# Performance work log

Measured on AMD Instinct MI355X. Metric: run time of the kernel, lower is better.

Reference implementation:

```python
import jax, jax.numpy as jnp
import numpy as np

B, Q, K = 4, 256, 1024
Q_SIZE, K_SIZE, V_SIZE, H = 256, 256, 256, 128
NEG = -1000000.0


def setup_inputs() -> dict:
    key = jax.random.key(0)
    ks = jax.random.split(key, 7)
    return {
        "queries": jax.random.normal(ks[0], (B, Q, Q_SIZE), dtype=jnp.float32),
        "keys": jax.random.normal(ks[1], (B, K, K_SIZE), dtype=jnp.float32),
        "values": jax.random.normal(ks[2], (B, K, V_SIZE), dtype=jnp.float32),
        "valid_lens": jax.random.randint(ks[3], (B,), 1, K + 1),
        # Linear weights stored torch-style: [out_features, in_features]
        "W_q": jax.random.normal(ks[4], (H, Q_SIZE), dtype=jnp.float32) * (1.0 / np.sqrt(Q_SIZE)),
        "W_k": jax.random.normal(ks[5], (H, K_SIZE), dtype=jnp.float32) * (1.0 / np.sqrt(K_SIZE)),
        "w_v": jax.random.normal(ks[6], (H,), dtype=jnp.float32) * (1.0 / np.sqrt(H)),
    }


def reference(queries, keys, values, valid_lens, W_q, W_k, w_v):
    # Projections (torch Linear: x @ W.T)
    q = jnp.einsum("bqi,hi->bqh", queries, W_q)  # [B,Q,H]
    k = jnp.einsum("bki,hi->bkh", keys, W_k)     # [B,K,H]
    # Broadcast add + tanh -> additive scores via dot with w_v
    feat = jnp.tanh(q[:, :, None, :] + k[:, None, :, :])  # [B,Q,K,H]
    scores = jnp.einsum("bqkh,h->bqk", feat, w_v)          # [B,Q,K]
    # masked_softmax: 1-D valid_lens broadcast over all query rows
    mask = jnp.arange(K)[None, None, :] < valid_lens[:, None, None]  # [B,1,K]
    scores = jnp.where(mask, scores, NEG)
    attn = jax.nn.softmax(scores, axis=-1)
    # dropout p=0.0 (eval): identity
    return jnp.einsum("bqk,bkv->bqv", attn, values)  # [B,Q,V]
```

## Files before the change

kernel.cpp:

```cpp
#include <hip/hip_runtime.h>
#include <math.h>

#define BQ   4
#define QN   256
#define KN   1024
#define DIN  256
#define HD   128

#define C2F   2.8853900817779268f
#define NL2E  (-2.8853900817779268f)

__global__ __launch_bounds__(256, 2) void proj_kernel(const float* __restrict__ queries,
                                                      const float* __restrict__ keys,
                                                      const float* __restrict__ W_q,
                                                      const float* __restrict__ W_k,
                                                      float* __restrict__ Eq,
                                                      float* __restrict__ EkT4) {
    __shared__ float xT[32][18];
    __shared__ float WT[32][136];

    const int t = threadIdx.x;
    const int row0 = blockIdx.x * 16;
    const bool is_q = row0 < BQ * QN;
    const float* x = is_q ? queries : keys;
    const float* W = is_q ? W_q : W_k;
    const int xr0 = is_q ? row0 : row0 - BQ * QN;

    const int h0 = (t & 31) * 4;
    const int r0 = (t >> 5) * 2;

    float acc[2][4];
#pragma unroll
    for (int r = 0; r < 2; r++)
#pragma unroll
        for (int c = 0; c < 4; c++) acc[r][c] = 0.f;

    for (int ks = 0; ks < DIN; ks += 32) {
        __syncthreads();
        if (t < 128) {
            const int r = t >> 3, k4 = (t & 7) * 4;
            float4 xv = *(const float4*)(x + (size_t)(xr0 + r) * DIN + ks + k4);
            xT[k4 + 0][r] = xv.x; xT[k4 + 1][r] = xv.y;
            xT[k4 + 2][r] = xv.z; xT[k4 + 3][r] = xv.w;
        }
#pragma unroll
        for (int u = 0; u < 4; u++) {
            const int h = (t >> 3) + 32 * u, k4 = (t & 7) * 4;
            float4 wv = *(const float4*)(W + (size_t)h * DIN + ks + k4);
            WT[k4 + 0][h] = wv.x; WT[k4 + 1][h] = wv.y;
            WT[k4 + 2][h] = wv.z; WT[k4 + 3][h] = wv.w;
        }
        __syncthreads();
#pragma unroll
        for (int kk = 0; kk < 32; kk++) {
            float2 xv = *(const float2*)&xT[kk][r0];
            float4 wv = *(const float4*)&WT[kk][h0];
            const float xr[2] = {xv.x, xv.y};
            const float wc[4] = {wv.x, wv.y, wv.z, wv.w};
#pragma unroll
            for (int r = 0; r < 2; r++)
#pragma unroll
                for (int c = 0; c < 4; c++)
                    acc[r][c] = __builtin_fmaf(xr[r], wc[c], acc[r][c]);
        }
    }

    if (is_q) {
#pragma unroll
        for (int r = 0; r < 2; r++) {
            float4 o;
            o.x = __builtin_amdgcn_exp2f(C2F * acc[r][0]);
            o.y = __builtin_amdgcn_exp2f(C2F * acc[r][1]);
            o.z = __builtin_amdgcn_exp2f(C2F * acc[r][2]);
            o.w = __builtin_amdgcn_exp2f(C2F * acc[r][3]);
            *(float4*)(Eq + (size_t)(row0 + r0 + r) * HD + h0) = o;
        }
    } else {
        const int krow = row0 - BQ * QN;
        const int b = krow >> 10, k0 = (krow & (KN - 1)) + r0;
        const int h4 = t & 31;
#pragma unroll
        for (int r = 0; r < 2; r++) {
            float4 o;
            o.x = __builtin_amdgcn_exp2f(C2F * acc[r][0]);
            o.y = __builtin_amdgcn_exp2f(C2F * acc[r][1]);
            o.z = __builtin_amdgcn_exp2f(C2F * acc[r][2]);
            o.w = __builtin_amdgcn_exp2f(C2F * acc[r][3]);
            *(float4*)(EkT4 + ((size_t)(b * 32 + h4) * KN + k0 + r) * 4) = o;
        }
    }
}

__global__ __launch_bounds__(256, 4) void score_kernel(const float* __restrict__ Eq,
                                                       const float* __restrict__ EkT4,
                                                       const int* __restrict__ valid_lens,
                                                       const float* __restrict__ w_v,
                                                       float* __restrict__ attn,
                                                       float* __restrict__ partial) {
    __shared__ float s_w[HD];
    __shared__ float s_pq[HD][8];
    __shared__ float s_part[2][8][128];
    __shared__ float s_red[4][4];

    const int blk = blockIdx.x;
    const int b = blk & 3;
    const int q0 = ((blk >> 2) & 31) * 8;
    const int c = blk >> 7;
    const int t = threadIdx.x;
    const int valid = valid_lens[b];
    float* pp = partial + (size_t)(b * QN + q0) * 8;

    if (c * 128 >= valid) {
        if (t < 8) pp[t * 8 + c] = 0.f;
        return;
    }

    const int kl = t & 127;
    const int hh = t >> 7;
    const int k = c * 128 + kl;

    if (t < HD) s_w[t] = w_v[t];
    {
        const int h = t & 127;
#pragma unroll
        for (int j = 0; j < 4; j++) {
            const int q = (t >> 7) * 4 + j;
            s_pq[h][q] = Eq[(size_t)(b * QN + q0 + q) * HD + h];
        }
    }
    __syncthreads();

    const float4* kcol = (const float4*)EkT4 + ((size_t)(b * 32 + hh * 16) * KN + k);
    float acc[8] = {0.f, 0.f, 0.f, 0.f, 0.f, 0.f, 0.f, 0.f};

#pragma unroll 4
    for (int i = 0; i < 16; i++) {
        float4 ek4 = kcol[(size_t)i * KN];
        const int hb = hh * 64 + i * 4;
        const float ekv[4] = {ek4.x, ek4.y, ek4.z, ek4.w};
#pragma unroll
        for (int j = 0; j < 4; j++) {
            const float ek = ekv[j];
            const float w = s_w[hb + j];
            float4 p0 = *(const float4*)&s_pq[hb + j][0];
            float4 p1 = *(const float4*)&s_pq[hb + j][4];
            acc[0] = __builtin_fmaf(w, __builtin_amdgcn_rcpf(__builtin_fmaf(ek, p0.x, 1.0f)), acc[0]);
            acc[1] = __builtin_fmaf(w, __builtin_amdgcn_rcpf(__builtin_fmaf(ek, p0.y, 1.0f)), acc[1]);
            acc[2] = __builtin_fmaf(w, __builtin_amdgcn_rcpf(__builtin_fmaf(ek, p0.z, 1.0f)), acc[2]);
            acc[3] = __builtin_fmaf(w, __builtin_amdgcn_rcpf(__builtin_fmaf(ek, p0.w, 1.0f)), acc[3]);
            acc[4] = __builtin_fmaf(w, __builtin_amdgcn_rcpf(__builtin_fmaf(ek, p1.x, 1.0f)), acc[4]);
            acc[5] = __builtin_fmaf(w, __builtin_amdgcn_rcpf(__builtin_fmaf(ek, p1.y, 1.0f)), acc[5]);
            acc[6] = __builtin_fmaf(w, __builtin_amdgcn_rcpf(__builtin_fmaf(ek, p1.z, 1.0f)), acc[6]);
            acc[7] = __builtin_fmaf(w, __builtin_amdgcn_rcpf(__builtin_fmaf(ek, p1.w, 1.0f)), acc[7]);
        }
    }

#pragma unroll
    for (int q = 0; q < 8; q++) s_part[hh][q][kl] = acc[q];
    __syncthreads();

    const int qb = (t >> 7) * 4;
    float* arow = attn + (size_t)(b * QN + q0 + qb) * KN + k;
    float psum[4];
#pragma unroll
    for (int j = 0; j < 4; j++) {
        const int q = qb + j;
        float tot = s_part[0][q][kl] + s_part[1][q][kl];
        float e = (k < valid) ? __builtin_amdgcn_exp2f(NL2E * tot) : 0.f;
        arow[(size_t)j * KN] = e;
#pragma unroll
        for (int off = 32; off > 0; off >>= 1) e += __shfl_xor(e, off, 64);
        psum[j] = e;
    }
    const int wv = t >> 6;
    if ((t & 63) == 0) {
#pragma unroll
        for (int j = 0; j < 4; j++) s_red[wv][j] = psum[j];
    }
    __syncthreads();
    if (t < 8) {
        const int q = t;
        float s = (q < 4) ? (s_red[0][q] + s_red[1][q])
                          : (s_red[2][q - 4] + s_red[3][q - 4]);
        pp[q * 8 + c] = s;
    }
}

__global__ __launch_bounds__(256, 2) void av_kernel(const float* __restrict__ attn,
                                                    const float* __restrict__ partial,
                                                    const float* __restrict__ values,
                                                    const int* __restrict__ valid_lens,
                                                    float* __restrict__ out) {
    __shared__ float s_aT[32][20];
    __shared__ float s_v[32][36];
    __shared__ float s_red[8][16][37];
    __shared__ float s_inv[16];

    const int blk = blockIdx.x;
    const int b = blk & 3;
    const int qt = (blk >> 2) & 15;
    const int vt = blk >> 6;
    const int t = threadIdx.x;
    const int q0 = qt * 16, v0 = vt * 32;
    const int valid = valid_lens[b];
    const int T = (valid + 31) >> 5;

    if (t < 16) {
        const float* pr = partial + (size_t)(b * QN + q0 + t) * 8;
        float4 pA = *(const float4*)pr;
        float4 pB = *(const float4*)(pr + 4);
        s_inv[t] = 1.0f / (pA.x + pA.y + pA.z + pA.w + pB.x + pB.y + pB.z + pB.w);
    }

    const int sr = t >> 3, sc = (t & 7) * 4;
    const float* abase = attn + (size_t)(b * QN + q0 + (sr & 15)) * KN + sc;
    const float* vbase = values + ((size_t)b * KN + sr) * DIN + v0 + sc;

    const int ks = t >> 5;
    const int qh = (t >> 3) & 3;
    const int vh = t & 7;

    float acc[4][4];
#pragma unroll
    for (int r = 0; r < 4; r++)
#pragma unroll
        for (int c = 0; c < 4; c++) acc[r][c] = 0.f;

    float4 ra = *(const float4*)abase;
    float4 rv = *(const float4*)vbase;

    for (int tile = 0; tile < T; tile++) {
        __syncthreads();
        if (t < 128) {
            s_aT[sc + 0][sr] = ra.x;
            s_aT[sc + 1][sr] = ra.y;
            s_aT[sc + 2][sr] = ra.z;
            s_aT[sc + 3][sr] = ra.w;
        }
        *(float4*)&s_v[sr][sc] = rv;
        __syncthreads();
        if (tile + 1 < T) {
            ra = *(const float4*)(abase + (tile + 1) * 32);
            rv = *(const float4*)(vbase + (size_t)(tile + 1) * 32 * DIN);
        }
#pragma unroll
        for (int i = 0; i < 4; i++) {
            const int kk = ks * 4 + i;
            float4 aq = *(const float4*)&s_aT[kk][qh * 4];
            float4 vv = *(const float4*)&s_v[kk][vh * 4];
            const float ar[4] = {aq.x, aq.y, aq.z, aq.w};
            const float vc[4] = {vv.x, vv.y, vv.z, vv.w};
#pragma unroll
            for (int r = 0; r < 4; r++)
#pragma unroll
                for (int c = 0; c < 4; c++)
                    acc[r][c] = __builtin_fmaf(ar[r], vc[c], acc[r][c]);
        }
    }

#pragma unroll
    for (int r = 0; r < 4; r++)
        *(float4*)&s_red[ks][qh * 4 + r][vh * 4] =
            make_float4(acc[r][0], acc[r][1], acc[r][2], acc[r][3]);
    __syncthreads();

    if (t < 128) {
        const int q = t >> 3, v4 = (t & 7) * 4;
        float4 o = {0.f, 0.f, 0.f, 0.f};
#pragma unroll
        for (int s = 0; s < 8; s++) {
            float4 r = *(const float4*)&s_red[s][q][v4];
            o.x += r.x; o.y += r.y; o.z += r.z; o.w += r.w;
        }
        const float inv = s_inv[q];
        o.x *= inv; o.y *= inv; o.z *= inv; o.w *= inv;
        *(float4*)(out + (size_t)(b * QN + q0 + q) * DIN + v0 + v4) = o;
    }
}

extern "C" void kernel_launch(void* const* d_in, const int* in_sizes, int n_in,
                              void* d_out, int out_size, void* d_ws, size_t ws_size,
                              hipStream_t stream) {
    const float* queries    = (const float*)d_in[0];
    const float* keys       = (const float*)d_in[1];
    const float* values     = (const float*)d_in[2];
    const int*   valid_lens = (const int*)d_in[3];
    const float* W_q        = (const float*)d_in[4];
    const float* W_k        = (const float*)d_in[5];
    const float* w_v        = (const float*)d_in[6];
    float* out = (float*)d_out;

    float* Eq      = (float*)d_ws;
    float* EkT4    = Eq + (size_t)BQ * QN * HD;
    float* attn    = EkT4 + (size_t)BQ * HD * KN;
    float* partial = attn + (size_t)BQ * QN * KN;

    proj_kernel<<<(BQ * QN + BQ * KN) / 16, 256, 0, stream>>>(queries, keys, W_q, W_k, Eq, EkT4);
    score_kernel<<<BQ * (QN / 8) * 8, 256, 0, stream>>>(Eq, EkT4, valid_lens, w_v, attn, partial);
    av_kernel<<<BQ * 16 * 8, 256, 0, stream>>>(attn, partial, values, valid_lens, out);
}
```

Before: 111.9 us.

## Compact score grid over valid key chunks with 64-key blocks and 4-way H split

```diff
diff --git a/kernel.cpp b/kernel.cpp
--- a/kernel.cpp
+++ b/kernel.cpp
@@ -99,90 +99,79 @@
                                                        float* __restrict__ partial) {
     __shared__ float s_w[HD];
     __shared__ float s_pq[HD][8];
-    __shared__ float s_part[2][8][128];
-    __shared__ float s_red[4][4];
-
-    const int blk = blockIdx.x;
-    const int b = blk & 3;
-    const int q0 = ((blk >> 2) & 31) * 8;
-    const int c = blk >> 7;
+    __shared__ float s_part[4][8][64];
+
+    const int v0 = valid_lens[0], v1 = valid_lens[1];
+    const int v2 = valid_lens[2], v3 = valid_lens[3];
+    const int e0 = 32 * ((v0 + 63) >> 6);
+    const int e1 = e0 + 32 * ((v1 + 63) >> 6);
+    const int e2 = e1 + 32 * ((v2 + 63) >> 6);
+    const int e3 = e2 + 32 * ((v3 + 63) >> 6);
+    const int j = blockIdx.x;
+    if (j >= e3) return;
+    int b, valid, jj;
+    if (j < e0)      { b = 0; valid = v0; jj = j; }
+    else if (j < e1) { b = 1; valid = v1; jj = j - e0; }
+    else if (j < e2) { b = 2; valid = v2; jj = j - e1; }
+    else             { b = 3; valid = v3; jj = j - e2; }
+    const int q0 = (jj & 31) * 8;
+    const int c  = jj >> 5;
+
     const int t = threadIdx.x;
-    const int valid = valid_lens[b];
-    float* pp = partial + (size_t)(b * QN + q0) * 8;
-
-    if (c * 128 >= valid) {
-        if (t < 8) pp[t * 8 + c] = 0.f;
-        return;
-    }
-
-    const int kl = t & 127;
-    const int hh = t >> 7;
-    const int k = c * 128 + kl;
+    const int l = t & 63;
+    const int w = t >> 6;
+    const int k = c * 64 + l;
 
     if (t < HD) s_w[t] = w_v[t];
     {
         const int h = t & 127;
 #pragma unroll
-        for (int j = 0; j < 4; j++) {
-            const int q = (t >> 7) * 4 + j;
+        for (int jq = 0; jq < 4; jq++) {
+            const int q = (t >> 7) * 4 + jq;
             s_pq[h][q] = Eq[(size_t)(b * QN + q0 + q) * HD + h];
         }
     }
     __syncthreads();
 
-    const float4* kcol = (const float4*)EkT4 + ((size_t)(b * 32 + hh * 16) * KN + k);
+    const float4* kcol = (const float4*)EkT4 + ((size_t)(b * 32 + w * 8) * KN + k);
     float acc[8] = {0.f, 0.f, 0.f, 0.f, 0.f, 0.f, 0.f, 0.f};
 
-#pragma unroll 4
-    for (int i = 0; i < 16; i++) {
+#pragma unroll
+    for (int i = 0; i < 8; i++) {
         float4 ek4 = kcol[(size_t)i * KN];
-        const int hb = hh * 64 + i * 4;
+        const int hb = w * 32 + i * 4;
         const float ekv[4] = {ek4.x, ek4.y, ek4.z, ek4.w};
 #pragma unroll
-        for (int j = 0; j < 4; j++) {
-            const float ek = ekv[j];
-            const float w = s_w[hb + j];
-            float4 p0 = *(const float4*)&s_pq[hb + j][0];
-            float4 p1 = *(const float4*)&s_pq[hb + j][4];
-            acc[0] = __builtin_fmaf(w, __builtin_amdgcn_rcpf(__builtin_fmaf(ek, p0.x, 1.0f)), acc[0]);
-            acc[1] = __builtin_fmaf(w, __builtin_amdgcn_rcpf(__builtin_fmaf(ek, p0.y, 1.0f)), acc[1]);
-            acc[2] = __builtin_fmaf(w, __builtin_amdgcn_rcpf(__builtin_fmaf(ek, p0.z, 1.0f)), acc[2]);
-            acc[3] = __builtin_fmaf(w, __builtin_amdgcn_rcpf(__builtin_fmaf(ek, p0.w, 1.0f)), acc[3]);
-            acc[4] = __builtin_fmaf(w, __builtin_amdgcn_rcpf(__builtin_fmaf(ek, p1.x, 1.0f)), acc[4]);
-            acc[5] = __builtin_fmaf(w, __builtin_amdgcn_rcpf(__builtin_fmaf(ek, p1.y, 1.0f)), acc[5]);
-            acc[6] = __builtin_fmaf(w, __builtin_amdgcn_rcpf(__builtin_fmaf(ek, p1.z, 1.0f)), acc[6]);
-            acc[7] = __builtin_fmaf(w, __builtin_amdgcn_rcpf(__builtin_fmaf(ek, p1.w, 1.0f)), acc[7]);
-        }
-    }
-
-#pragma unroll
-    for (int q = 0; q < 8; q++) s_part[hh][q][kl] = acc[q];
+        for (int jh = 0; jh < 4; jh++) {
+            const float ek = ekv[jh];
+            const float wv = s_w[hb + jh];
+            float4 p0 = *(const float4*)&s_pq[hb + jh][0];
+            float4 p1 = *(const float4*)&s_pq[hb + jh][4];
+            acc[0] = __builtin_fmaf(wv, __builtin_amdgcn_rcpf(__builtin_fmaf(ek, p0.x, 1.0f)), acc[0]);
+            acc[1] = __builtin_fmaf(wv, __builtin_amdgcn_rcpf(__builtin_fmaf(ek, p0.y, 1.0f)), acc[1]);
+            acc[2] = __builtin_fmaf(wv, __builtin_amdgcn_rcpf(__builtin_fmaf(ek, p0.z, 1.0f)), acc[2]);
+            acc[3] = __builtin_fmaf(wv, __builtin_amdgcn_rcpf(__builtin_fmaf(ek, p0.w, 1.0f)), acc[3]);
+            acc[4] = __builtin_fmaf(wv, __builtin_amdgcn_rcpf(__builtin_fmaf(ek, p1.x, 1.0f)), acc[4]);
+            acc[5] = __builtin_fmaf(wv, __builtin_amdgcn_rcpf(__builtin_fmaf(ek, p1.y, 1.0f)), acc[5]);
+            acc[6] = __builtin_fmaf(wv, __builtin_amdgcn_rcpf(__builtin_fmaf(ek, p1.z, 1.0f)), acc[6]);
+            acc[7] = __builtin_fmaf(wv, __builtin_amdgcn_rcpf(__builtin_fmaf(ek, p1.w, 1.0f)), acc[7]);
+        }
+    }
+
+#pragma unroll
+    for (int q = 0; q < 8; q++) s_part[w][q][l] = acc[q];
     __syncthreads();
 
-    const int qb = (t >> 7) * 4;
-    float* arow = attn + (size_t)(b * QN + q0 + qb) * KN + k;
-    float psum[4];
-#pragma unroll
-    for (int j = 0; j < 4; j++) {
-        const int q = qb + j;
-        float tot = s_part[0][q][kl] + s_part[1][q][kl];
+#pragma unroll
+    for (int jq = 0; jq < 2; jq++) {
+        const int q = w * 2 + jq;
+        float tot = s_part[0][q][l] + s_part[1][q][l] + s_part[2][q][l] + s_part[3][q][l];
         float e = (k < valid) ? __builtin_amdgcn_exp2f(NL2E * tot) : 0.f;
-        arow[(size_t)j * KN] = e;
-#pragma unroll
-        for (int off = 32; off > 0; off >>= 1) e += __shfl_xor(e, off, 64);
-        psum[j] = e;
-    }
-    const int wv = t >> 6;
-    if ((t & 63) == 0) {
-#pragma unroll
-        for (int j = 0; j < 4; j++) s_red[wv][j] = psum[j];
-    }
-    __syncthreads();
-    if (t < 8) {
-        const int q = t;
-        float s = (q < 4) ? (s_red[0][q] + s_red[1][q])
-                          : (s_red[2][q - 4] + s_red[3][q - 4]);
-        pp[q * 8 + c] = s;
+        attn[(size_t)(b * QN + q0 + q) * KN + k] = e;
+        float r = e;
+#pragma unroll
+        for (int off = 32; off > 0; off >>= 1) r += __shfl_xor(r, off, 64);
+        if (l == 0) partial[(size_t)(b * QN + q0 + q) * 16 + c] = r;
     }
 }
 
@@ -206,10 +195,11 @@
     const int T = (valid + 31) >> 5;
 
     if (t < 16) {
-        const float* pr = partial + (size_t)(b * QN + q0 + t) * 8;
-        float4 pA = *(const float4*)pr;
-        float4 pB = *(const float4*)(pr + 4);
-        s_inv[t] = 1.0f / (pA.x + pA.y + pA.z + pA.w + pB.x + pB.y + pB.z + pB.w);
+        const float* pr = partial + (size_t)(b * QN + q0 + t) * 16;
+        const int nc = (valid + 63) >> 6;
+        float s = 0.f;
+        for (int cc = 0; cc < nc; cc++) s += pr[cc];
+        s_inv[t] = 1.0f / s;
     }
 
     const int sr = t >> 3, sc = (t & 7) * 4;
@@ -296,6 +286,6 @@
     float* partial = attn + (size_t)BQ * QN * KN;
 
     proj_kernel<<<(BQ * QN + BQ * KN) / 16, 256, 0, stream>>>(queries, keys, W_q, W_k, Eq, EkT4);
-    score_kernel<<<BQ * (QN / 8) * 8, 256, 0, stream>>>(Eq, EkT4, valid_lens, w_v, attn, partial);
+    score_kernel<<<BQ * (QN / 8) * 16, 256, 0, stream>>>(Eq, EkT4, valid_lens, w_v, attn, partial);
     av_kernel<<<BQ * 16 * 8, 256, 0, stream>>>(attn, partial, values, valid_lens, out);
 }
```

After: 105.8 us. -5.5%, faster.
